# Kernel tuning notes

Measured on AMD Instinct MI355X. Metric: run time of the kernel, lower is better.

Reference implementation:

```python
import jax, jax.numpy as jnp
import numpy as np

LN_EPS = 1e-5

def _linear(x, W, b):
    # torch nn.Linear equivalent with W stored as [in, out]
    return jnp.einsum('bsd,de->bse', x, W) + b

def setup_inputs() -> dict:
    key = jax.random.key(0)
    ks = jax.random.split(key, 8)
    B, S, D = 4, 4096, 1024
    scale = 0.02
    inp = {
        'x': jax.random.normal(ks[0], (B, S, D), dtype=jnp.float32),
        'Wk': jax.random.normal(ks[1], (D, D), dtype=jnp.float32) * scale,
        'bk': jnp.zeros((D,), jnp.float32),
        'Wv': jax.random.normal(ks[2], (D, D), dtype=jnp.float32) * scale,
        'bv': jnp.zeros((D,), jnp.float32),
        'Wq': jax.random.normal(ks[3], (D, D), dtype=jnp.float32) * scale,
        'bq': jnp.zeros((D,), jnp.float32),
        'Wkp': jax.random.normal(ks[4], (D, D), dtype=jnp.float32) * scale,
        'bkp': jnp.zeros((D,), jnp.float32),
        'Wqp': jax.random.normal(ks[5], (D, D), dtype=jnp.float32) * scale,
        'bqp': jnp.zeros((D,), jnp.float32),
        'ln_g': jnp.ones((D,), jnp.float32),
        'ln_b': jnp.zeros((D,), jnp.float32),
        'Wo': jax.random.normal(ks[6], (D, D), dtype=jnp.float32) * scale,
        'bo': jnp.zeros((D,), jnp.float32),
        'idx': jax.random.permutation(ks[7], S)[:32].astype(jnp.int32),
        'chunk_size': 64,
    }
    return inp

def _ortho_loss(kc, ks_, idx):
    # sample rows, pairwise Re(conj(z_i) z_j) = cos_i cos_j + sin_i sin_j
    B, _, D = kc.shape
    n = idx.shape[0]
    cs = kc[:, idx, :]                                # [B, n, D]
    sn = ks_[:, idx, :]
    dot = cs[:, :, None, :] * cs[:, None, :, :] + sn[:, :, None, :] * sn[:, None, :, :]  # [B,n,n,D]
    mask = (~jnp.eye(n, dtype=bool))[None, :, :, None].astype(dot.dtype)
    denom = jnp.float32(n * (n - 1)) * D + 1e-6       # mask.sum() * dim + eps
    return jnp.sum(dot * dot * mask) / denom

def reference(x, Wk, bk, Wv, bv, Wq, bq, Wkp, bkp, Wqp, bqp, ln_g, ln_b, Wo, bo, idx, chunk_size):
    B, S, D = x.shape
    key = _linear(x, Wk, bk)
    value = _linear(x, Wv, bv)
    query = _linear(x, Wq, bq)
    key_phase = _linear(key, Wkp, bkp)
    query_phase = _linear(query, Wqp, bqp)
    kc, ksin = jnp.cos(key_phase), jnp.sin(key_phase)
    qc, qsin = jnp.cos(query_phase), jnp.sin(query_phase)
    ortho = _ortho_loss(kc, ksin, idx)
    br = value * kc
    bi = value * ksin
    pad = (-S) % chunk_size
    if pad > 0:
        pw = ((0, 0), (0, pad), (0, 0))
        br = jnp.pad(br, pw); bi = jnp.pad(bi, pw)
        qc = jnp.pad(qc, pw); qsin = jnp.pad(qsin, pw)
    P = S + pad
    nc = P // chunk_size
    shp = (B, nc, chunk_size, D)
    mem_r = jnp.cumsum(br.reshape(shp), axis=2)
    mem_i = jnp.cumsum(bi.reshape(shp), axis=2)
    retrieved = mem_r * qc.reshape(shp) + mem_i * qsin.reshape(shp)
    retrieved = retrieved.reshape(B, P, D)[:, :S]
    retrieved = retrieved / jnp.sqrt(jnp.float32(S))
    mu = jnp.mean(retrieved, axis=-1, keepdims=True)
    var = jnp.var(retrieved, axis=-1, keepdims=True)
    ln = (retrieved - mu) * jax.lax.rsqrt(var + LN_EPS) * ln_g + ln_b
    out = x + _linear(ln, Wo, bo)
    return out, ortho
```

## Files before the change

### kernel.cpp

```cpp
#include <hip/hip_runtime.h>
#include <math.h>

#define D_DIM 1024
#define S_DIM 4096
#define B_DIM 4
#define CHUNK 64
#define NC (S_DIM / CHUNK)
#define M_DIM (B_DIM * S_DIM)
#define MD ((size_t)M_DIM * D_DIM)

typedef __bf16 bf16_t;
typedef __attribute__((ext_vector_type(8))) __bf16 bf16x8;
typedef __attribute__((ext_vector_type(4))) __bf16 bf16x4;
typedef __attribute__((ext_vector_type(2))) __bf16 bf16x2;
typedef __attribute__((ext_vector_type(4))) float f32x4;

__device__ __forceinline__ void async_copy16(const void* g, void* lds) {
  __builtin_amdgcn_global_load_lds(
      (const __attribute__((address_space(1))) unsigned int*)g,
      (__attribute__((address_space(3))) unsigned int*)lds, 16, 0, 0);
}

template <int MODE>
__global__ __launch_bounds__(256) void gemm_mfma(const bf16_t* __restrict__ A,
                                                 const bf16_t* __restrict__ Bt,
                                                 const float* __restrict__ bias,
                                                 const float* __restrict__ res,
                                                 float* __restrict__ Cf,
                                                 bf16_t* __restrict__ Cb) {
  constexpr int K = D_DIM;
  constexpr int NB_N = (MODE == 0) ? 24 : 8;
  constexpr int NB_M = (MODE == 3) ? 16 : 128;
  __shared__ bf16_t sm[4 * 4096];

  const int bid = blockIdx.x;
  const int xcd = bid & 7;
  const int slot = bid >> 3;
  const int bm = (xcd * (NB_M / 8) + slot / NB_N) * 128;
  const int bn = (slot % NB_N) * 128;

  const int tid = threadIdx.x;
  const int lane = tid & 63;
  const int wave = tid >> 6;
  const int wm = wave & 1, wn = wave >> 1;
  const int quad = lane >> 4;
  const int l15 = lane & 15;

  bf16_t* As0 = sm;
  bf16_t* As1 = sm + 4096;
  bf16_t* Bs0 = sm + 8192;
  bf16_t* Bs1 = sm + 12288;

  const bf16_t* BtP = Bt;
  if (MODE == 3) BtP = Bt + (size_t)(bm >> 10) * D_DIM * D_DIM;

  f32x4 acc[4][4];
#pragma unroll
  for (int i = 0; i < 4; i++)
#pragma unroll
    for (int j = 0; j < 4; j++) acc[i][j] = (f32x4){0.f, 0.f, 0.f, 0.f};

  const int e0 = tid, e1 = tid + 256;
  const int wofs = wave * 512;
  const bf16_t* a0 = A + (size_t)(bm + (e0 >> 2)) * K + (e0 & 3) * 8;
  const bf16_t* a1 = A + (size_t)(bm + (e1 >> 2)) * K + (e1 & 3) * 8;
  const bf16_t* b0 = BtP + (size_t)(bn + (e0 >> 2)) * K + (e0 & 3) * 8;
  const bf16_t* b1 = BtP + (size_t)(bn + (e1 >> 2)) * K + (e1 & 3) * 8;

  for (int k0 = 0; k0 < K; k0 += 64) {
    async_copy16(a0 + k0, As0 + wofs);
    async_copy16(a1 + k0, As0 + 2048 + wofs);
    async_copy16(b0 + k0, Bs0 + wofs);
    async_copy16(b1 + k0, Bs0 + 2048 + wofs);
    async_copy16(a0 + k0 + 32, As1 + wofs);
    async_copy16(a1 + k0 + 32, As1 + 2048 + wofs);
    async_copy16(b0 + k0 + 32, Bs1 + wofs);
    async_copy16(b1 + k0 + 32, Bs1 + 2048 + wofs);
    __syncthreads();

#pragma unroll
    for (int h = 0; h < 2; h++) {
      const bf16_t* Ah = h ? As1 : As0;
      const bf16_t* Bh = h ? Bs1 : Bs0;
      bf16x8 af[4], bfr[4];
#pragma unroll
      for (int t = 0; t < 4; t++) {
        af[t] = *(const bf16x8*)(Ah + (size_t)(wm * 64 + t * 16 + l15) * 32 + quad * 8);
        bfr[t] = *(const bf16x8*)(Bh + (size_t)(wn * 64 + t * 16 + l15) * 32 + quad * 8);
      }
#pragma unroll
      for (int mt = 0; mt < 4; mt++)
#pragma unroll
        for (int nt = 0; nt < 4; nt++)
          acc[mt][nt] =
              __builtin_amdgcn_mfma_f32_16x16x32_bf16(af[mt], bfr[nt], acc[mt][nt], 0, 0, 0);
    }
    __syncthreads();
  }

  const int baserow = bm + wm * 64;
  const int basecol = bn + wn * 64 + l15;
#pragma unroll
  for (int mt = 0; mt < 4; mt++) {
#pragma unroll
    for (int nt = 0; nt < 4; nt++) {
      const int n = basecol + nt * 16;
      const float bv = (MODE == 3) ? 0.f : bias[n];
#pragma unroll
      for (int r = 0; r < 4; r++) {
        const int m = baserow + mt * 16 + quad * 4 + r;
        float v = acc[mt][nt][r] + bv;
        if (MODE == 2) {
          v += res[(size_t)m * D_DIM + n];
          Cf[(size_t)m * D_DIM + n] = v;
        } else if (MODE == 0) {
          Cb[(size_t)(bn >> 10) * MD + (size_t)m * D_DIM + (n & 1023)] = (bf16_t)v;
        } else {
          Cb[(size_t)(bm >> 10) * D_DIM * D_DIM + (size_t)(m & 1023) * D_DIM + n] =
              (bf16_t)v;
        }
      }
    }
  }
}

__global__ __launch_bounds__(256) void prep_all(
    const float* __restrict__ s0, const float* __restrict__ s1,
    const float* __restrict__ s2, const float* __restrict__ s3,
    bf16_t* __restrict__ d0, bf16_t* __restrict__ d1,
    bf16_t* __restrict__ d2, bf16_t* __restrict__ d3,
    const float* __restrict__ x, const float* __restrict__ Wk,
    const float* __restrict__ Wq, bf16_t* __restrict__ xb,
    bf16_t* __restrict__ wkb, bf16_t* __restrict__ wqb) {
  const int z = blockIdx.z;
  if (z < 4) {
    const float* srcs[4] = {s0, s1, s2, s3};
    bf16_t* dsts[4] = {d0, d1, d2, d3};
    const float* W = srcs[z];
    bf16_t* Wt = dsts[z];
    __shared__ float tile[32][33];
    const int bx = blockIdx.x * 32;
    const int by = blockIdx.y * 32;
    const int tx = threadIdx.x & 31, ty = threadIdx.x >> 5;
#pragma unroll
    for (int r = 0; r < 32; r += 8)
      tile[ty + r][tx] = W[(size_t)(by + ty + r) * D_DIM + bx + tx];
    __syncthreads();
#pragma unroll
    for (int r = 0; r < 32; r += 8)
      Wt[(size_t)(bx + ty + r) * D_DIM + by + tx] = (bf16_t)tile[tx][ty + r];
  } else {
    size_t i = ((size_t)(z - 4) * 1024 + blockIdx.y * 32 + blockIdx.x) * 256 +
               threadIdx.x;
    const float* src;
    bf16_t* dst;
    size_t off;
    if (i < 4194304) { src = x; dst = xb; off = i; }
    else if (i < 4456448) { src = Wk; dst = wkb; off = i - 4194304; }
    else { src = Wq; dst = wqb; off = i - 4456448; }
    const float4 v = ((const float4*)src)[off];
    bf16x4 o;
    o[0] = (bf16_t)v.x; o[1] = (bf16_t)v.y; o[2] = (bf16_t)v.z; o[3] = (bf16_t)v.w;
    ((bf16x4*)dst)[off] = o;
  }
}

__global__ __launch_bounds__(256) void fused_bias_k(
    const float* __restrict__ bv, const float* __restrict__ bk,
    const float* __restrict__ bkp, const float* __restrict__ bq,
    const float* __restrict__ bqp, const float* __restrict__ Wkp,
    const float* __restrict__ Wqp, float* __restrict__ fb) {
  const int n = blockIdx.x * 256 + threadIdx.x;
  const int t = n >> 10, c = n & 1023;
  if (t == 0) {
    fb[n] = bv[c];
    return;
  }
  const float* W = (t == 1) ? Wkp : Wqp;
  const float* b1 = (t == 1) ? bk : bq;
  const float* b2 = (t == 1) ? bkp : bqp;
  float s = b2[c];
#pragma unroll 8
  for (int k = 0; k < D_DIM; k++) s = fmaf(b1[k], W[(size_t)k * D_DIM + c], s);
  fb[n] = s;
}

__global__ __launch_bounds__(512) void scan_ln(const bf16_t* __restrict__ vb,
                                               const bf16_t* __restrict__ kp,
                                               const bf16_t* __restrict__ qp,
                                               const float* __restrict__ g,
                                               const float* __restrict__ bl,
                                               bf16_t* __restrict__ outb) {
  __shared__ bf16_t retl[32 * 1024];
  const int chunk = blockIdx.x;
  const int b = blockIdx.y;
  const int tid = threadIdx.x;
  const int lane = tid & 63, wave = tid >> 6;
  const int c = tid * 2;
  const size_t base = ((size_t)(b * S_DIM + chunk * CHUNK)) * D_DIM + c;
  float2 mr = {0.f, 0.f}, mi = {0.f, 0.f};
  const float inv = 0.015625f;

  for (int half = 0; half < 2; half++) {
    for (int s8 = 0; s8 < 32; s8++) {
      const int s = half * 32 + s8;
      const size_t off = base + (size_t)s * D_DIM;
      bf16x2 v2 = *(const bf16x2*)(vb + off);
      bf16x2 k2 = *(const bf16x2*)(kp + off);
      bf16x2 q2 = *(const bf16x2*)(qp + off);
      float sk, ck, sq, cq;
      __sincosf((float)k2[0], &sk, &ck);
      mr.x = fmaf((float)v2[0], ck, mr.x);
      mi.x = fmaf((float)v2[0], sk, mi.x);
      __sincosf((float)k2[1], &sk, &ck);
      mr.y = fmaf((float)v2[1], ck, mr.y);
      mi.y = fmaf((float)v2[1], sk, mi.y);
      bf16x2 r;
      __sincosf((float)q2[0], &sq, &cq);
      r[0] = (bf16_t)((mr.x * cq + mi.x * sq) * inv);
      __sincosf((float)q2[1], &sq, &cq);
      r[1] = (bf16_t)((mr.y * cq + mi.y * sq) * inv);
      *(bf16x2*)(retl + s8 * 1024 + c) = r;
    }
    __syncthreads();
#pragma unroll
    for (int j = 0; j < 4; j++) {
      const int r8 = wave * 4 + j;
      const int col0 = lane * 16;
      const bf16x8 va = *(const bf16x8*)(retl + r8 * 1024 + col0);
      const bf16x8 vb8 = *(const bf16x8*)(retl + r8 * 1024 + col0 + 8);
      float vf[16];
#pragma unroll
      for (int k = 0; k < 8; k++) { vf[k] = (float)va[k]; vf[8 + k] = (float)vb8[k]; }
      float s = 0.f, ss = 0.f;
#pragma unroll
      for (int k = 0; k < 16; k++) { s += vf[k]; ss += vf[k] * vf[k]; }
#pragma unroll
      for (int o = 32; o > 0; o >>= 1) {
        s += __shfl_down(s, o);
        ss += __shfl_down(ss, o);
      }
      s = __shfl(s, 0);
      ss = __shfl(ss, 0);
      const float mu = s * (1.f / D_DIM);
      const float var = ss * (1.f / D_DIM) - mu * mu;
      const float rs = 1.f / sqrtf(var + 1e-5f);
      const int m = b * S_DIM + chunk * CHUNK + half * 32 + r8;
      bf16x8 o1, o2;
#pragma unroll
      for (int q = 0; q < 4; q++) {
        const float4 gv = *(const float4*)(g + col0 + 4 * q);
        const float4 bv = *(const float4*)(bl + col0 + 4 * q);
        const int kbase = 4 * q;
        float r0 = (vf[kbase + 0] - mu) * rs * gv.x + bv.x;
        float r1 = (vf[kbase + 1] - mu) * rs * gv.y + bv.y;
        float r2 = (vf[kbase + 2] - mu) * rs * gv.z + bv.z;
        float r3 = (vf[kbase + 3] - mu) * rs * gv.w + bv.w;
        if (q < 2) {
          o1[kbase + 0] = (bf16_t)r0; o1[kbase + 1] = (bf16_t)r1;
          o1[kbase + 2] = (bf16_t)r2; o1[kbase + 3] = (bf16_t)r3;
        } else {
          o2[kbase - 8] = (bf16_t)r0; o2[kbase - 7] = (bf16_t)r1;
          o2[kbase - 6] = (bf16_t)r2; o2[kbase - 5] = (bf16_t)r3;
        }
      }
      *(bf16x8*)(outb + (size_t)m * D_DIM + col0) = o1;
      *(bf16x8*)(outb + (size_t)m * D_DIM + col0 + 8) = o2;
    }
    __syncthreads();
  }
}

__global__ __launch_bounds__(256) void ortho_partial(const bf16_t* __restrict__ kp,
                                                     const int* __restrict__ idx,
                                                     float* __restrict__ partial) {
  const int i = blockIdx.x;
  const int b = blockIdx.y;
  const int ri = idx[i];
  const bf16x4 ab = *(const bf16x4*)(kp + ((size_t)b * S_DIM + ri) * D_DIM + threadIdx.x * 4);
  float a0 = (float)ab[0], a1 = (float)ab[1], a2 = (float)ab[2], a3 = (float)ab[3];
  float sum = 0.f;
  for (int j = 0; j < 32; j++) {
    if (j == i) continue;
    const int rj = idx[j];
    const bf16x4 cb = *(const bf16x4*)(kp + ((size_t)b * S_DIM + rj) * D_DIM + threadIdx.x * 4);
    float d0 = __cosf(a0 - (float)cb[0]);
    float d1 = __cosf(a1 - (float)cb[1]);
    float d2 = __cosf(a2 - (float)cb[2]);
    float d3 = __cosf(a3 - (float)cb[3]);
    sum += d0 * d0 + d1 * d1 + d2 * d2 + d3 * d3;
  }
#pragma unroll
  for (int o = 32; o > 0; o >>= 1) sum += __shfl_down(sum, o);
  __shared__ float red[4];
  if ((threadIdx.x & 63) == 0) red[threadIdx.x >> 6] = sum;
  __syncthreads();
  if (threadIdx.x == 0) partial[b * 32 + i] = red[0] + red[1] + red[2] + red[3];
}

__global__ void ortho_final(const float* __restrict__ partial, float* __restrict__ outp) {
  if (threadIdx.x == 0) {
    double s = 0.0;
    for (int t = 0; t < 128; t++) s += (double)partial[t];
    const double denom = (double)(32 * 31) * 1024.0 + 1e-6;
    outp[0] = (float)(s / denom);
  }
}

extern "C" void kernel_launch(void* const* d_in, const int* in_sizes, int n_in,
                              void* d_out, int out_size, void* d_ws, size_t ws_size,
                              hipStream_t stream) {
  const float* x = (const float*)d_in[0];
  const float* Wk = (const float*)d_in[1];
  const float* bk = (const float*)d_in[2];
  const float* Wv = (const float*)d_in[3];
  const float* bv = (const float*)d_in[4];
  const float* Wq = (const float*)d_in[5];
  const float* bq = (const float*)d_in[6];
  const float* Wkp = (const float*)d_in[7];
  const float* bkp = (const float*)d_in[8];
  const float* Wqp = (const float*)d_in[9];
  const float* bqp = (const float*)d_in[10];
  const float* ln_g = (const float*)d_in[11];
  const float* ln_b = (const float*)d_in[12];
  const float* Wo = (const float*)d_in[13];
  const float* bo = (const float*)d_in[14];
  const int* idx = (const int*)d_in[15];

  float* out = (float*)d_out;
  float* ortho_out = out + MD;

  char* ws = (char*)d_ws;
  const size_t MB = 1024 * 1024;
  bf16_t* QKVT = (bf16_t*)(ws + 0 * MB);
  bf16_t* WoT = (bf16_t*)(ws + 6 * MB);
  bf16_t* WkpT2 = (bf16_t*)(ws + 8 * MB);
  float* fbias = (float*)(ws + 12 * MB);
  float* partial = (float*)(ws + 12 * MB + 16 * 1024);
  bf16_t* Wkqb = (bf16_t*)(ws + 13 * MB);
  bf16_t* xb = (bf16_t*)(ws + 32 * MB);
  bf16_t* mega_out = (bf16_t*)(ws + 64 * MB);
  bf16_t* kp_b = mega_out + MD;
  bf16_t* qp_b = mega_out + 2 * MD;
  bf16_t* lnb = (bf16_t*)(ws + 32 * MB);

  prep_all<<<dim3(32, 32, 22), 256, 0, stream>>>(
      Wv, Wkp, Wqp, Wo, QKVT, WkpT2, WkpT2 + (size_t)D_DIM * D_DIM, WoT,
      x, Wk, Wq, xb, Wkqb, Wkqb + (size_t)D_DIM * D_DIM);
  gemm_mfma<3><<<128, 256, 0, stream>>>(WkpT2, Wkqb, nullptr, nullptr, nullptr,
                                        QKVT + (size_t)D_DIM * D_DIM);
  fused_bias_k<<<12, 256, 0, stream>>>(bv, bk, bkp, bq, bqp, Wkp, Wqp, fbias);

  gemm_mfma<0><<<24 * 128, 256, 0, stream>>>(xb, QKVT, fbias, nullptr, nullptr,
                                             mega_out);
  ortho_partial<<<dim3(32, B_DIM), 256, 0, stream>>>(kp_b, idx, partial);
  scan_ln<<<dim3(NC, B_DIM), 512, 0, stream>>>(mega_out, kp_b, qp_b, ln_g, ln_b,
                                               lnb);
  gemm_mfma<2><<<8 * 128, 256, 0, stream>>>(lnb, WoT, bo, x, out, nullptr);
  ortho_final<<<1, 64, 0, stream>>>(partial, ortho_out);
}
```

Baseline: 453.0 us.

## Replace 128x128 GEMMs with 256x256-tile 8-wave pipelined MFMA kernel

Adds a new GEMM kernel that uses 256x256 output tiles with 512 threads (8 waves), double-buffered LDS stages fed by async global-to-LDS copies, and interleaved LDS reads and MFMA groups with explicit barriers and priority hints. The large QKV/phase projection GEMM and the output projection GEMM now use it instead of the 128x128 kernel. The aim is more data reuse per LDS byte and better overlap of memory traffic with matrix math. In exchange it raises register and LDS pressure (64K bf16 of LDS per block) and cuts grid size, which may leave CUs underused on the smaller output GEMM.

```diff
diff --git a/kernel.cpp b/kernel.cpp
--- a/kernel.cpp
+++ b/kernel.cpp
@@ -19,6 +19,177 @@
   __builtin_amdgcn_global_load_lds(
       (const __attribute__((address_space(1))) unsigned int*)g,
       (__attribute__((address_space(3))) unsigned int*)lds, 16, 0, 0);
+}
+
+#define SB __builtin_amdgcn_s_barrier()
+#define WAIT_LGKM do { asm volatile("s_waitcnt lgkmcnt(0)" ::: "memory"); \
+                       __builtin_amdgcn_sched_barrier(0); } while (0)
+#define PRIO1 __builtin_amdgcn_s_setprio(1)
+#define PRIO0 __builtin_amdgcn_s_setprio(0)
+
+template <int MODE>
+__global__ __launch_bounds__(512, 2) void gemm256(const bf16_t* __restrict__ A,
+                                                  const bf16_t* __restrict__ Bt,
+                                                  const float* __restrict__ bias,
+                                                  const float* __restrict__ res,
+                                                  float* __restrict__ Cf,
+                                                  bf16_t* __restrict__ Cb) {
+  constexpr int K = D_DIM;
+  constexpr int NB_N = (MODE == 0) ? 12 : 4;
+  __shared__ bf16_t sm[65536];
+
+  const int bid = blockIdx.x;
+  const int xcd = bid & 7;
+  const int slot = bid >> 3;
+  const int bm = (xcd * 8 + slot / NB_N) * 256;
+  const int bn = (slot % NB_N) * 256;
+
+  const int tid = threadIdx.x;
+  const int lane = tid & 63;
+  const int wave = tid >> 6;
+  const int wm = wave >> 2;
+  const int wn = wave & 3;
+  const int quad = lane >> 4;
+  const int l15 = lane & 15;
+  const int lane8 = lane * 8;
+  const int bg = (wn & 1) * 4;
+
+  const int c0 = tid, c1 = tid + 512;
+#define ROWOF(c) ((((c) >> 7) & 7) * 16 + ((c) & 15))
+#define KGOF(c) ((((c) >> 6) & 1) * 4 + (((c) >> 4) & 3))
+  const bf16_t* gA0 = A + (size_t)(bm + ROWOF(c0)) * K + KGOF(c0) * 8;
+  const bf16_t* gA1 = A + (size_t)(bm + ROWOF(c1)) * K + KGOF(c1) * 8;
+  const bf16_t* gB0 = Bt + (size_t)(bn + ROWOF(c0)) * K + KGOF(c0) * 8;
+  const bf16_t* gB1 = Bt + (size_t)(bn + ROWOF(c1)) * K + KGOF(c1) * 8;
+
+  bf16_t* stA0 = sm + wave * 512;
+  bf16_t* stB0 = sm + 16384 + wave * 512;
+  bf16_t* stA1 = sm + 32768 + wave * 512;
+  bf16_t* stB1 = sm + 49152 + wave * 512;
+  const bf16_t* A0p = sm + wm * 8192 + lane8;
+  const bf16_t* B0p = sm + 16384 + (wn >> 1) * 8192 + lane8;
+  const bf16_t* A1p = sm + 32768 + wm * 8192 + lane8;
+  const bf16_t* B1p = sm + 49152 + (wn >> 1) * 8192 + lane8;
+
+#define STG(gp0, gp1, kofs, db, hx)                                        \
+  do {                                                                     \
+    async_copy16(gp0 + (size_t)(hx)*131072 + (kofs), (db) + (hx)*8192);    \
+    async_copy16(gp1 + (size_t)(hx)*131072 + (kofs), (db) + (hx)*8192 + 4096); \
+  } while (0)
+
+  f32x4 acc[8][4];
+#pragma unroll
+  for (int i = 0; i < 8; i++)
+#pragma unroll
+    for (int j = 0; j < 4; j++) acc[i][j] = (f32x4){0.f, 0.f, 0.f, 0.f};
+
+  bf16x8 af[4][2], bl[2][2], bh[2][2];
+
+#define RDA(P, MS)                                                         \
+  _Pragma("unroll") for (int m = 0; m < 4; ++m) {                          \
+    af[m][0] = *(const bf16x8*)((P) + (((MS) + m) * 2 + 0) * 512);         \
+    af[m][1] = *(const bf16x8*)((P) + (((MS) + m) * 2 + 1) * 512);         \
+  }
+#define RDB(P, DST, NS)                                                    \
+  _Pragma("unroll") for (int n = 0; n < 2; ++n) {                          \
+    DST[n][0] = *(const bf16x8*)((P) + (((NS) + n) * 2 + 0) * 512);        \
+    DST[n][1] = *(const bf16x8*)((P) + (((NS) + n) * 2 + 1) * 512);        \
+  }
+#define MFQ(MB, NB, BB)                                                    \
+  do {                                                                     \
+    PRIO1;                                                                 \
+    _Pragma("unroll") for (int m = 0; m < 4; ++m)                          \
+        _Pragma("unroll") for (int n = 0; n < 2; ++n) {                    \
+      acc[(MB) + m][(NB) + n] = __builtin_amdgcn_mfma_f32_16x16x32_bf16(   \
+          af[m][0], BB[n][0], acc[(MB) + m][(NB) + n], 0, 0, 0);           \
+      acc[(MB) + m][(NB) + n] = __builtin_amdgcn_mfma_f32_16x16x32_bf16(   \
+          af[m][1], BB[n][1], acc[(MB) + m][(NB) + n], 0, 0, 0);           \
+    }                                                                      \
+    PRIO0;                                                                 \
+  } while (0)
+
+  STG(gB0, gB1, 0, stB0, 0);
+  STG(gB0, gB1, 0, stB0, 1);
+  STG(gA0, gA1, 0, stA0, 0);
+  STG(gA0, gA1, 0, stA0, 1);
+  STG(gB0, gB1, 64, stB1, 0);
+  STG(gB0, gB1, 64, stB1, 1);
+  asm volatile("s_waitcnt vmcnt(4)" ::: "memory");
+  SB;
+
+  for (int i = 0; i < 8; ++i) {
+    const size_t kA1 = (size_t)(2 * i + 1) * 64;
+    const size_t kN = (size_t)(2 * i + 2) * 64;
+    const bool pf = (i < 7);
+
+    RDA(A0p, 0);
+    RDB(B0p, bl, bg);
+    STG(gA0, gA1, kA1, stA1, 0);
+    SB; WAIT_LGKM; MFQ(0, 0, bl); SB;
+
+    RDB(B0p, bh, bg + 2);
+    STG(gA0, gA1, kA1, stA1, 1);
+    SB; WAIT_LGKM; MFQ(0, 2, bh); SB;
+
+    RDA(A0p, 4);
+    if (pf) STG(gB0, gB1, kN, stB0, 0);
+    SB; WAIT_LGKM; MFQ(4, 2, bh); SB;
+
+    if (pf) STG(gB0, gB1, kN, stB0, 1);
+    SB; WAIT_LGKM; MFQ(4, 0, bl);
+    if (pf) { asm volatile("s_waitcnt vmcnt(4)" ::: "memory"); }
+    else    { asm volatile("s_waitcnt vmcnt(0)" ::: "memory"); }
+    SB;
+
+    RDA(A1p, 0);
+    RDB(B1p, bl, bg);
+    if (pf) STG(gA0, gA1, kN, stA0, 0);
+    SB; WAIT_LGKM; MFQ(0, 0, bl); SB;
+
+    RDB(B1p, bh, bg + 2);
+    if (pf) STG(gA0, gA1, kN, stA0, 1);
+    SB; WAIT_LGKM; MFQ(0, 2, bh); SB;
+
+    RDA(A1p, 4);
+    if (pf) STG(gB0, gB1, kN + 64, stB1, 0);
+    SB; WAIT_LGKM; MFQ(4, 2, bh); SB;
+
+    if (pf) STG(gB0, gB1, kN + 64, stB1, 1);
+    SB; WAIT_LGKM; MFQ(4, 0, bl);
+    if (pf) { asm volatile("s_waitcnt vmcnt(4)" ::: "memory"); }
+    else    { asm volatile("s_waitcnt vmcnt(0)" ::: "memory"); }
+    SB;
+  }
+  __builtin_amdgcn_sched_barrier(0);
+
+  const int baserow = bm + wm * 128;
+  const int basecol = bn + wn * 64 + l15;
+#pragma unroll
+  for (int nf = 0; nf < 4; ++nf) {
+    const int n = basecol + nf * 16;
+    const float bv = bias[n];
+#pragma unroll
+    for (int mf = 0; mf < 8; ++mf) {
+#pragma unroll
+      for (int r = 0; r < 4; ++r) {
+        const int m = baserow + mf * 16 + quad * 4 + r;
+        float v = acc[mf][nf][r] + bv;
+        if (MODE == 2) {
+          v += res[(size_t)m * D_DIM + n];
+          Cf[(size_t)m * D_DIM + n] = v;
+        } else {
+          Cb[(size_t)(n >> 10) * MD + (size_t)m * D_DIM + (n & 1023)] =
+              (bf16_t)v;
+        }
+      }
+    }
+  }
+#undef ROWOF
+#undef KGOF
+#undef STG
+#undef RDA
+#undef RDB
+#undef MFQ
 }
 
 template <int MODE>
@@ -351,11 +522,11 @@
                                         QKVT + (size_t)D_DIM * D_DIM);
   fused_bias_k<<<12, 256, 0, stream>>>(bv, bk, bkp, bq, bqp, Wkp, Wqp, fbias);
 
-  gemm_mfma<0><<<24 * 128, 256, 0, stream>>>(xb, QKVT, fbias, nullptr, nullptr,
-                                             mega_out);
+  gemm256<0><<<768, 512, 0, stream>>>(xb, QKVT, fbias, nullptr, nullptr,
+                                      mega_out);
   ortho_partial<<<dim3(32, B_DIM), 256, 0, stream>>>(kp_b, idx, partial);
   scan_ln<<<dim3(NC, B_DIM), 512, 0, stream>>>(mega_out, kp_b, qp_b, ln_g, ln_b,
                                                lnb);
-  gemm_mfma<2><<<8 * 128, 256, 0, stream>>>(lnb, WoT, bo, x, out, nullptr);
+  gemm256<2><<<256, 512, 0, stream>>>(lnb, WoT, bo, x, out, nullptr);
   ortho_final<<<1, 64, 0, stream>>>(partial, ortho_out);
 }
```

After: 477.3 us. 1.05x slower.
